# Kernel tuning notes

Hardware: AMD Instinct MI355X
Metric: run time of the kernel (lower is better)

Reference implementation:

```python
import jax, jax.numpy as jnp
import numpy as np

B, D, K = 16384, 4096, 14
EPS = 1e-12  # torch F.normalize eps


def _normalize(x):
    n = jnp.sqrt(jnp.sum(x * x, axis=-1, keepdims=True))
    return x / jnp.maximum(n, EPS)


def setup_inputs() -> dict:
    key = jax.random.key(0)
    ks = jax.random.split(key, 9)
    image_feat = jax.random.normal(ks[0], (B, D), dtype=jnp.float32)
    text_feat = jax.random.normal(ks[1], (B, D), dtype=jnp.float32)
    disease_labels = jax.random.randint(ks[2], (B, K), 0, 2, dtype=jnp.int32)
    # nn.Linear default init: U(-1/sqrt(D), 1/sqrt(D))
    lim = 1.0 / np.sqrt(D)
    Wv = jax.random.uniform(ks[3], (D, D), jnp.float32, -lim, lim)
    bv = jax.random.uniform(ks[4], (D,), jnp.float32, -lim, lim)
    Wt = jax.random.uniform(ks[5], (D, D), jnp.float32, -lim, lim)
    bt = jax.random.uniform(ks[6], (D,), jnp.float32, -lim, lim)
    prototypes = jax.random.normal(ks[7], (K, D), dtype=jnp.float32) * 0.02
    cooccur = np.eye(K, dtype=np.float32)
    for i, j in [(1, 3), (0, 9), (7, 9)]:
        cooccur[i, j] = 0.7
        cooccur[j, i] = 0.7
    cooccurrence = jnp.asarray(cooccur)
    return {
        "image_feat": image_feat, "text_feat": text_feat,
        "disease_labels": disease_labels,
        "Wv": Wv, "bv": bv, "Wt": Wt, "bt": bt,
        "prototypes": prototypes, "cooccurrence": cooccurrence,
    }


def reference(image_feat, text_feat, disease_labels, Wv, bv, Wt, bt, prototypes, cooccurrence):
    labels_f = disease_labels.astype(jnp.float32)  # [B, K]
    v = _normalize(image_feat @ Wv.T + bv)          # [B, D]
    t = _normalize(text_feat @ Wt.T + bt)           # [B, D]
    p = _normalize(prototypes)                      # [K, D]
    v_sim = v @ p.T                                 # [B, K]
    t_sim = t @ p.T                                 # [B, K]
    # Coalition value is linear in the mask and the sampled coalitions differ
    # only at index i, so every Monte Carlo marginal equals this closed form
    # exactly (randomness cancels in value_with - value_without).
    shapley = 0.5 * (v_sim + t_sim) * labels_f      # [B, K]
    batch_cooccur = (labels_f.T @ labels_f) / labels_f.shape[0]  # [K, K]
    learned = jax.nn.sigmoid(cooccurrence)
    cooccur_loss = jnp.mean((learned - jax.lax.stop_gradient(batch_cooccur)) ** 2)
    return shapley, prototypes, cooccur_loss
```

## Files before the change

kernel.cpp:

```cpp
#include <hip/hip_runtime.h>

typedef __bf16 bf16x8 __attribute__((ext_vector_type(8)));
typedef float f32x4 __attribute__((ext_vector_type(4)));
typedef unsigned short u16;
typedef unsigned int u32;

#define D_DIM 4096
#define B_ROWS 16384
#define K_CLS 14
#define M_TOT 32768

__device__ __forceinline__ u32 f2bf(float f) {
    u32 u = __float_as_uint(f);
    return (u + 0x7FFFu + ((u >> 16) & 1u)) >> 16;
}
__device__ __forceinline__ float bfl(u32 u) { return __uint_as_float(u << 16); }
__device__ __forceinline__ float bfh(u32 u) { return __uint_as_float(u & 0xFFFF0000u); }

typedef __attribute__((address_space(3))) void lds_void;
typedef __attribute__((address_space(1))) void glb_void;

__device__ __forceinline__ void g2lds16(const void* g, void* l) {
    __builtin_amdgcn_global_load_lds(
        reinterpret_cast<glb_void*>(reinterpret_cast<uintptr_t>(g)),
        reinterpret_cast<lds_void*>(reinterpret_cast<uintptr_t>(l)),
        16, 0, 0);
}

__global__ void cast_bf16(const float* __restrict__ src, u16* __restrict__ dst, int n4) {
    int i = blockIdx.x * blockDim.x + threadIdx.x;
    int stride = gridDim.x * blockDim.x;
    for (; i < n4; i += stride) {
        float4 a = ((const float4*)src)[i];
        uint2 o;
        o.x = f2bf(a.x) | (f2bf(a.y) << 16);
        o.y = f2bf(a.z) | (f2bf(a.w) << 16);
        ((uint2*)dst)[i] = o;
    }
}

__global__ void proto_norm(const float* __restrict__ P, u16* __restrict__ pTbf,
                           float* __restrict__ outProto) {
    const int k = blockIdx.x;
    const int tid = threadIdx.x;
    float ss = 0.f;
    for (int d = tid; d < D_DIM; d += 256) {
        float v = P[k * D_DIM + d];
        ss += v * v;
    }
    for (int off = 32; off; off >>= 1) ss += __shfl_down(ss, off);
    __shared__ float red[4];
    if ((tid & 63) == 0) red[tid >> 6] = ss;
    __syncthreads();
    float tot = red[0] + red[1] + red[2] + red[3];
    float inv = 1.0f / fmaxf(sqrtf(tot), 1e-12f);
    for (int d = tid; d < D_DIM; d += 256) {
        float v = P[k * D_DIM + d];
        outProto[k * D_DIM + d] = v;
        pTbf[(size_t)d * 16 + k] = (u16)f2bf(v * inv);
    }
}

__global__ void cooccur_bc(const int* __restrict__ L, float* __restrict__ bc) {
    const int i = blockIdx.x / K_CLS, j = blockIdx.x % K_CLS;
    int s = 0;
    for (int b = threadIdx.x; b < B_ROWS; b += 256)
        s += L[b * K_CLS + i] * L[b * K_CLS + j];
    for (int off = 32; off; off >>= 1) s += __shfl_down(s, off);
    __shared__ int red[4];
    if ((threadIdx.x & 63) == 0) red[threadIdx.x >> 6] = s;
    __syncthreads();
    if (threadIdx.x == 0)
        bc[blockIdx.x] = (float)(red[0] + red[1] + red[2] + red[3]) / (float)B_ROWS;
}

__global__ void cooccur_loss(const float* __restrict__ C, const float* __restrict__ bc,
                             float* __restrict__ out) {
    const int t = threadIdx.x;
    float d2 = 0.f;
    if (t < K_CLS * K_CLS) {
        float s = 1.0f / (1.0f + expf(-C[t]));
        float d = s - bc[t];
        d2 = d * d;
    }
    for (int off = 32; off; off >>= 1) d2 += __shfl_down(d2, off);
    __shared__ float red[4];
    if ((t & 63) == 0) red[t >> 6] = d2;
    __syncthreads();
    if (t == 0) out[0] = (red[0] + red[1] + red[2] + red[3]) / (float)(K_CLS * K_CLS);
}

__global__ __launch_bounds__(256) void gemm_bt(
    const u16* __restrict__ Xbf,
    const u16* __restrict__ Wbf,
    const float* __restrict__ bv, const float* __restrict__ bt,
    u16* __restrict__ Ybf)
{
    __shared__ __align__(16) u16 As[128 * 32];
    __shared__ __align__(16) u16 Bs[128 * 32];

    const int tid = threadIdx.x;
    const int wave = tid >> 6, lane = tid & 63;
    const int bn0 = blockIdx.x * 128;
    const int bm0 = blockIdx.y * 128;
    const int half = (bm0 >= B_ROWS) ? 1 : 0;
    const u16* Wsel = Wbf + (size_t)half * D_DIM * D_DIM;
    const float* bias = half ? bt : bv;

    const int srA = lane >> 2;
    const int sc  = (lane & 3) * 8;
    const int g0 = wave * 2, g1 = wave * 2 + 1;
    const u16* Ag = Xbf + (size_t)bm0 * D_DIM;
    const u16* Bg = Wsel + (size_t)bn0 * D_DIM;
    const u16* ga0 = Ag + (size_t)(g0 * 16 + srA) * D_DIM + sc;
    const u16* ga1 = Ag + (size_t)(g1 * 16 + srA) * D_DIM + sc;
    const u16* gb0 = Bg + (size_t)(g0 * 16 + srA) * D_DIM + sc;
    const u16* gb1 = Bg + (size_t)(g1 * 16 + srA) * D_DIM + sc;
    u16* la0 = &As[g0 * 512]; u16* la1 = &As[g1 * 512];
    u16* lb0 = &Bs[g0 * 512]; u16* lb1 = &Bs[g1 * 512];

    const int waveM = wave >> 1, waveN = wave & 1;
    const int mlane = lane & 15, quad = lane >> 4;
    const u16* Ar = &As[(waveM * 64 + mlane) * 32 + quad * 8];
    const u16* Br = &Bs[(waveN * 64 + mlane) * 32 + quad * 8];

    f32x4 acc[4][4] = {};

    for (int k0 = 0; k0 < D_DIM; k0 += 32) {
        __syncthreads();
        g2lds16(ga0 + k0, la0);
        g2lds16(ga1 + k0, la1);
        g2lds16(gb0 + k0, lb0);
        g2lds16(gb1 + k0, lb1);
        __syncthreads();
        bf16x8 a[4], b[4];
#pragma unroll
        for (int mi = 0; mi < 4; mi++) a[mi] = *(const bf16x8*)(Ar + mi * 16 * 32);
#pragma unroll
        for (int ni = 0; ni < 4; ni++) b[ni] = *(const bf16x8*)(Br + ni * 16 * 32);
#pragma unroll
        for (int mi = 0; mi < 4; mi++)
#pragma unroll
            for (int ni = 0; ni < 4; ni++)
                acc[mi][ni] = __builtin_amdgcn_mfma_f32_16x16x32_bf16(
                    a[mi], b[ni], acc[mi][ni], 0, 0, 0);
    }

#pragma unroll
    for (int ni = 0; ni < 4; ni++) {
        const int col = bn0 + waveN * 64 + ni * 16 + mlane;
        const float bcol = bias[col];
#pragma unroll
        for (int mi = 0; mi < 4; mi++) {
            f32x4 v = acc[mi][ni];
#pragma unroll
            for (int r = 0; r < 4; r++) {
                const int row = bm0 + waveM * 64 + mi * 16 + quad * 4 + r;
                Ybf[(size_t)row * D_DIM + col] = (u16)f2bf(v[r] + bcol);
            }
        }
    }
}

__global__ __launch_bounds__(256) void simproj(
    const u16* __restrict__ Ybf, const u16* __restrict__ pTbf,
    float* __restrict__ sim)
{
    const int tid = threadIdx.x;
    const int wave = tid >> 6, lane = tid & 63;
    const int r0 = blockIdx.x * 16 + wave * 4;
    const u16* Y0 = Ybf + (size_t)r0 * D_DIM;

    float acc[4][15];
#pragma unroll
    for (int r = 0; r < 4; r++)
#pragma unroll
        for (int k = 0; k < 15; k++) acc[r][k] = 0.f;

#pragma unroll 2
    for (int i = 0; i < 64; i++) {
        const int d = lane + i * 64;
        const uint4* pq = (const uint4*)(pTbf + (size_t)d * 16);
        const uint4 q0 = pq[0], q1 = pq[1];
        const float p[14] = { bfl(q0.x), bfh(q0.x), bfl(q0.y), bfh(q0.y),
                              bfl(q0.z), bfh(q0.z), bfl(q0.w), bfh(q0.w),
                              bfl(q1.x), bfh(q1.x), bfl(q1.y), bfh(q1.y),
                              bfl(q1.z), bfh(q1.z) };
#pragma unroll
        for (int r = 0; r < 4; r++) {
            const float yv = bfl((u32)Y0[(size_t)r * D_DIM + d]);
            acc[r][14] += yv * yv;
#pragma unroll
            for (int k = 0; k < 14; k++) acc[r][k] += yv * p[k];
        }
    }
#pragma unroll
    for (int r = 0; r < 4; r++)
#pragma unroll
        for (int k = 0; k < 15; k++) {
            float v = acc[r][k];
            v += __shfl_xor(v, 1);  v += __shfl_xor(v, 2);  v += __shfl_xor(v, 4);
            v += __shfl_xor(v, 8);  v += __shfl_xor(v, 16); v += __shfl_xor(v, 32);
            acc[r][k] = v;
        }
    if (lane == 0) {
#pragma unroll
        for (int r = 0; r < 4; r++) {
            const float inv = 1.0f / fmaxf(sqrtf(acc[r][14]), 1e-12f);
#pragma unroll
            for (int k = 0; k < 14; k++)
                sim[(size_t)(r0 + r) * K_CLS + k] = acc[r][k] * inv;
        }
    }
}

__global__ void finalize(const float* __restrict__ sim, const int* __restrict__ L,
                         float* __restrict__ out) {
    const int t = blockIdx.x * 256 + threadIdx.x;
    if (t >= B_ROWS * K_CLS) return;
    out[t] = 0.5f * (sim[t] + sim[t + B_ROWS * K_CLS]) * (float)L[t];
}

extern "C" void kernel_launch(void* const* d_in, const int* in_sizes, int n_in,
                              void* d_out, int out_size, void* d_ws, size_t ws_size,
                              hipStream_t stream) {
    const float* image  = (const float*)d_in[0];
    const float* text   = (const float*)d_in[1];
    const int*   labels = (const int*)d_in[2];
    const float* Wv     = (const float*)d_in[3];
    const float* bv     = (const float*)d_in[4];
    const float* Wt     = (const float*)d_in[5];
    const float* bt     = (const float*)d_in[6];
    const float* protos = (const float*)d_in[7];
    const float* cooc   = (const float*)d_in[8];
    float* out = (float*)d_out;

    const size_t OFF_X   = 0;
    const size_t OFF_W   = 268435456ull;
    const size_t OFF_Y   = 335544320ull;
    const size_t OFF_PT  = 603979776ull;
    const size_t OFF_SIM = 604110848ull;
    const size_t OFF_BC  = 605945856ull;
    const size_t NEED    = 605946640ull;
    if (ws_size < NEED) return;

    char* ws = (char*)d_ws;
    u16*   Xbf  = (u16*)(ws + OFF_X);
    u16*   Wbf  = (u16*)(ws + OFF_W);
    u16*   Ybf  = (u16*)(ws + OFF_Y);
    u16*   pTbf = (u16*)(ws + OFF_PT);
    float* sim  = (float*)(ws + OFF_SIM);
    float* bc   = (float*)(ws + OFF_BC);

    cast_bf16<<<4096, 256, 0, stream>>>(image, Xbf, (B_ROWS * D_DIM) / 4);
    cast_bf16<<<4096, 256, 0, stream>>>(text, Xbf + (size_t)B_ROWS * D_DIM, (B_ROWS * D_DIM) / 4);
    cast_bf16<<<2048, 256, 0, stream>>>(Wv, Wbf, (D_DIM * D_DIM) / 4);
    cast_bf16<<<2048, 256, 0, stream>>>(Wt, Wbf + (size_t)D_DIM * D_DIM, (D_DIM * D_DIM) / 4);

    proto_norm<<<K_CLS, 256, 0, stream>>>(protos, pTbf, out + B_ROWS * K_CLS);
    cooccur_bc<<<K_CLS * K_CLS, 256, 0, stream>>>(labels, bc);
    cooccur_loss<<<1, 256, 0, stream>>>(cooc, bc, out + B_ROWS * K_CLS + K_CLS * D_DIM);

    gemm_bt<<<dim3(D_DIM / 128, M_TOT / 128), 256, 0, stream>>>(Xbf, Wbf, bv, bt, Ybf);

    simproj<<<M_TOT / 16, 256, 0, stream>>>(Ybf, pTbf, sim);

    finalize<<<(B_ROWS * K_CLS + 255) / 256, 256, 0, stream>>>(sim, labels, out);
}
```

Baseline: 1.968 ms.

## Rewrite bf16 GEMM with 256x256 double-buffered tiles and fuse finalize into simproj

The GEMM moves from 128x128 tiles with BK=32, which synchronised twice per k-step, to 256x256 tiles with BK=64 across 8 waves. It double-buffers LDS with async global-to-LDS loads issued two tiles ahead, XOR-swizzles the LDS layout to avoid bank conflicts, and uses setprio-guarded MFMA phases plus a grid swizzle for L2 locality. The aim is to raise arithmetic intensity and hide memory latency behind MFMA work. The simproj kernel now processes image and text rows together and writes the final labelled output directly, which removes the separate finalize kernel and the sim buffer. The larger tile uses 128KB of LDS and more registers, which may limit occupancy.

```diff
diff --git a/kernel.cpp b/kernel.cpp
--- a/kernel.cpp
+++ b/kernel.cpp
@@ -90,86 +90,161 @@
     if (t == 0) out[0] = (red[0] + red[1] + red[2] + red[3]) / (float)(K_CLS * K_CLS);
 }
 
-__global__ __launch_bounds__(256) void gemm_bt(
+#define BK 64
+#define NKT (D_DIM / BK)
+#define TILE_E (256 * 64)
+
+#define STAGE(ABUF, BBUF, k0) do {                                             \
+    _Pragma("unroll")                                                          \
+    for (int i_ = 0; i_ < 4; i_++)                                             \
+        g2lds16(Apan + gOff[i_] + (k0), (ABUF) + lOff[i_]);                    \
+    _Pragma("unroll")                                                          \
+    for (int i_ = 0; i_ < 4; i_++)                                             \
+        g2lds16(Bpan + gOff[i_] + (k0), (BBUF) + lOff[i_]);                    \
+} while (0)
+
+#define LOAD_B(BBUF) do {                                                      \
+    _Pragma("unroll")                                                          \
+    for (int ni_ = 0; ni_ < 4; ni_++) {                                        \
+        bfr[ni_][0] = *(const bf16x8*)((BBUF) + bBase + ni_ * 16 * BK + so0);  \
+        bfr[ni_][1] = *(const bf16x8*)((BBUF) + bBase + ni_ * 16 * BK + so1);  \
+    }                                                                          \
+} while (0)
+
+#define LOAD_A(ABUF, q) do {                                                   \
+    _Pragma("unroll")                                                          \
+    for (int s_ = 0; s_ < 2; s_++) {                                           \
+        afr[s_][0] = *(const bf16x8*)((ABUF) + aBase + ((q) * 32 + s_ * 16) * BK + so0); \
+        afr[s_][1] = *(const bf16x8*)((ABUF) + aBase + ((q) * 32 + s_ * 16) * BK + so1); \
+    }                                                                          \
+} while (0)
+
+#define MFMA_PHASE(q) do {                                                     \
+    __builtin_amdgcn_s_setprio(1);                                             \
+    _Pragma("unroll")                                                          \
+    for (int s_ = 0; s_ < 2; s_++)                                             \
+    _Pragma("unroll")                                                          \
+    for (int ni_ = 0; ni_ < 4; ni_++) {                                        \
+        acc[(q) * 2 + s_][ni_] = __builtin_amdgcn_mfma_f32_16x16x32_bf16(      \
+            afr[s_][0], bfr[ni_][0], acc[(q) * 2 + s_][ni_], 0, 0, 0);         \
+        acc[(q) * 2 + s_][ni_] = __builtin_amdgcn_mfma_f32_16x16x32_bf16(      \
+            afr[s_][1], bfr[ni_][1], acc[(q) * 2 + s_][ni_], 0, 0, 0);         \
+    }                                                                          \
+    __builtin_amdgcn_s_setprio(0);                                             \
+} while (0)
+
+#define PHASE0(ABUF, BBUF) do { LOAD_B(BBUF); LOAD_A(ABUF, 0);                 \
+    __builtin_amdgcn_s_barrier();                                              \
+    asm volatile("s_waitcnt lgkmcnt(0)" ::: "memory");                         \
+    __builtin_amdgcn_sched_barrier(0);                                         \
+    MFMA_PHASE(0);                                                             \
+    __builtin_amdgcn_s_barrier(); } while (0)
+
+#define PHASEQ(ABUF, q) do { LOAD_A(ABUF, q);                                  \
+    __builtin_amdgcn_s_barrier();                                              \
+    asm volatile("s_waitcnt lgkmcnt(0)" ::: "memory");                         \
+    __builtin_amdgcn_sched_barrier(0);                                         \
+    MFMA_PHASE(q);                                                             \
+    __builtin_amdgcn_s_barrier(); } while (0)
+
+#define TILE_BODY(ABUF, BBUF, t) do {                                          \
+    bf16x8 bfr[4][2], afr[2][2];                                               \
+    PHASE0(ABUF, BBUF);                                                        \
+    PHASEQ(ABUF, 1);                                                           \
+    PHASEQ(ABUF, 2);                                                           \
+    PHASEQ(ABUF, 3);                                                           \
+    __builtin_amdgcn_sched_barrier(0);                                         \
+    if ((t) + 2 < NKT) {                                                       \
+        STAGE(ABUF, BBUF, ((t) + 2) * BK);                                     \
+        asm volatile("s_waitcnt vmcnt(8)" ::: "memory");                       \
+    } else if ((t) + 1 < NKT) {                                                \
+        asm volatile("s_waitcnt vmcnt(0)" ::: "memory");                       \
+    }                                                                          \
+    __builtin_amdgcn_sched_barrier(0);                                         \
+    __builtin_amdgcn_s_barrier();                                              \
+} while (0)
+
+__global__ __launch_bounds__(512, 2) void gemm_bt(
     const u16* __restrict__ Xbf,
     const u16* __restrict__ Wbf,
     const float* __restrict__ bv, const float* __restrict__ bt,
     u16* __restrict__ Ybf)
 {
-    __shared__ __align__(16) u16 As[128 * 32];
-    __shared__ __align__(16) u16 Bs[128 * 32];
+    __shared__ __align__(16) u16 lds[4 * TILE_E];
+    u16* const As0 = lds;
+    u16* const As1 = lds + TILE_E;
+    u16* const Bs0 = lds + 2 * TILE_E;
+    u16* const Bs1 = lds + 3 * TILE_E;
 
     const int tid = threadIdx.x;
     const int wave = tid >> 6, lane = tid & 63;
-    const int bn0 = blockIdx.x * 128;
-    const int bm0 = blockIdx.y * 128;
+
+    const int bid = blockIdx.x;
+    const int swzb = (bid & 7) * 256 + (bid >> 3);
+    const int bn0 = (swzb & 15) * 256;
+    const int bm0 = (swzb >> 4) * 256;
     const int half = (bm0 >= B_ROWS) ? 1 : 0;
-    const u16* Wsel = Wbf + (size_t)half * D_DIM * D_DIM;
+    const u16* __restrict__ Apan = Xbf + (size_t)bm0 * D_DIM;
+    const u16* __restrict__ Bpan = Wbf + (size_t)half * D_DIM * D_DIM
+                                       + (size_t)bn0 * D_DIM;
     const float* bias = half ? bt : bv;
 
-    const int srA = lane >> 2;
-    const int sc  = (lane & 3) * 8;
-    const int g0 = wave * 2, g1 = wave * 2 + 1;
-    const u16* Ag = Xbf + (size_t)bm0 * D_DIM;
-    const u16* Bg = Wsel + (size_t)bn0 * D_DIM;
-    const u16* ga0 = Ag + (size_t)(g0 * 16 + srA) * D_DIM + sc;
-    const u16* ga1 = Ag + (size_t)(g1 * 16 + srA) * D_DIM + sc;
-    const u16* gb0 = Bg + (size_t)(g0 * 16 + srA) * D_DIM + sc;
-    const u16* gb1 = Bg + (size_t)(g1 * 16 + srA) * D_DIM + sc;
-    u16* la0 = &As[g0 * 512]; u16* la1 = &As[g1 * 512];
-    u16* lb0 = &Bs[g0 * 512]; u16* lb1 = &Bs[g1 * 512];
-
-    const int waveM = wave >> 1, waveN = wave & 1;
+    const int lrow = lane >> 3;
+    const int lslot = ((lane & 7) ^ lrow) * 8;
+    size_t gOff[4];
+    int lOff[4];
+#pragma unroll
+    for (int i = 0; i < 4; i++) {
+        const int c = wave * 4 + i;
+        gOff[i] = (size_t)(c * 8 + lrow) * D_DIM + lslot;
+        lOff[i] = c * 512;
+    }
+
+    const int wm = wave >> 2, wn = wave & 3;
     const int mlane = lane & 15, quad = lane >> 4;
-    const u16* Ar = &As[(waveM * 64 + mlane) * 32 + quad * 8];
-    const u16* Br = &Bs[(waveN * 64 + mlane) * 32 + quad * 8];
-
-    f32x4 acc[4][4] = {};
-
-    for (int k0 = 0; k0 < D_DIM; k0 += 32) {
-        __syncthreads();
-        g2lds16(ga0 + k0, la0);
-        g2lds16(ga1 + k0, la1);
-        g2lds16(gb0 + k0, lb0);
-        g2lds16(gb1 + k0, lb1);
-        __syncthreads();
-        bf16x8 a[4], b[4];
-#pragma unroll
-        for (int mi = 0; mi < 4; mi++) a[mi] = *(const bf16x8*)(Ar + mi * 16 * 32);
-#pragma unroll
-        for (int ni = 0; ni < 4; ni++) b[ni] = *(const bf16x8*)(Br + ni * 16 * 32);
-#pragma unroll
-        for (int mi = 0; mi < 4; mi++)
-#pragma unroll
-            for (int ni = 0; ni < 4; ni++)
-                acc[mi][ni] = __builtin_amdgcn_mfma_f32_16x16x32_bf16(
-                    a[mi], b[ni], acc[mi][ni], 0, 0, 0);
+    const int lswz = lane & 7;
+    const int so0 = (quad ^ lswz) * 8;
+    const int so1 = ((4 + quad) ^ lswz) * 8;
+    const int aBase = (wm * 128 + mlane) * BK;
+    const int bBase = (wn * 64 + mlane) * BK;
+
+    f32x4 acc[8][4] = {};
+
+    STAGE(As0, Bs0, 0);
+    STAGE(As1, Bs1, BK);
+    asm volatile("s_waitcnt vmcnt(8)" ::: "memory");
+    __builtin_amdgcn_sched_barrier(0);
+    __builtin_amdgcn_s_barrier();
+
+    for (int tt = 0; tt < NKT; tt += 2) {
+        TILE_BODY(As0, Bs0, tt);
+        TILE_BODY(As1, Bs1, tt + 1);
     }
 
 #pragma unroll
     for (int ni = 0; ni < 4; ni++) {
-        const int col = bn0 + waveN * 64 + ni * 16 + mlane;
+        const int col = bn0 + wn * 64 + ni * 16 + mlane;
         const float bcol = bias[col];
 #pragma unroll
-        for (int mi = 0; mi < 4; mi++) {
+        for (int mi = 0; mi < 8; mi++) {
             f32x4 v = acc[mi][ni];
-#pragma unroll
-            for (int r = 0; r < 4; r++) {
-                const int row = bm0 + waveM * 64 + mi * 16 + quad * 4 + r;
-                Ybf[(size_t)row * D_DIM + col] = (u16)f2bf(v[r] + bcol);
-            }
+            const size_t rb = (size_t)(bm0 + wm * 128 + mi * 16 + quad * 4) * D_DIM + col;
+#pragma unroll
+            for (int r = 0; r < 4; r++)
+                Ybf[rb + (size_t)r * D_DIM] = (u16)f2bf(v[r] + bcol);
         }
     }
 }
 
 __global__ __launch_bounds__(256) void simproj(
     const u16* __restrict__ Ybf, const u16* __restrict__ pTbf,
-    float* __restrict__ sim)
+    const int* __restrict__ L, float* __restrict__ out)
 {
     const int tid = threadIdx.x;
     const int wave = tid >> 6, lane = tid & 63;
-    const int r0 = blockIdx.x * 16 + wave * 4;
-    const u16* Y0 = Ybf + (size_t)r0 * D_DIM;
+    const int r0 = blockIdx.x * 8 + wave * 2;
+    const u16* Yi = Ybf + (size_t)r0 * D_DIM;
+    const u16* Yt = Yi + (size_t)B_ROWS * D_DIM;
 
     float acc[4][15];
 #pragma unroll
@@ -186,12 +261,16 @@
                               bfl(q0.z), bfh(q0.z), bfl(q0.w), bfh(q0.w),
                               bfl(q1.x), bfh(q1.x), bfl(q1.y), bfh(q1.y),
                               bfl(q1.z), bfh(q1.z) };
+        float yv[4];
+        yv[0] = bfl((u32)Yi[d]);
+        yv[1] = bfl((u32)Yi[D_DIM + d]);
+        yv[2] = bfl((u32)Yt[d]);
+        yv[3] = bfl((u32)Yt[D_DIM + d]);
 #pragma unroll
         for (int r = 0; r < 4; r++) {
-            const float yv = bfl((u32)Y0[(size_t)r * D_DIM + d]);
-            acc[r][14] += yv * yv;
-#pragma unroll
-            for (int k = 0; k < 14; k++) acc[r][k] += yv * p[k];
+            acc[r][14] += yv[r] * yv[r];
+#pragma unroll
+            for (int k = 0; k < 14; k++) acc[r][k] += yv[r] * p[k];
         }
     }
 #pragma unroll
@@ -205,20 +284,17 @@
         }
     if (lane == 0) {
 #pragma unroll
-        for (int r = 0; r < 4; r++) {
-            const float inv = 1.0f / fmaxf(sqrtf(acc[r][14]), 1e-12f);
-#pragma unroll
-            for (int k = 0; k < 14; k++)
-                sim[(size_t)(r0 + r) * K_CLS + k] = acc[r][k] * inv;
+        for (int rr = 0; rr < 2; rr++) {
+            const float iv = 1.0f / fmaxf(sqrtf(acc[rr][14]), 1e-12f);
+            const float it = 1.0f / fmaxf(sqrtf(acc[2 + rr][14]), 1e-12f);
+#pragma unroll
+            for (int k = 0; k < 14; k++) {
+                const int idx = (r0 + rr) * K_CLS + k;
+                out[idx] = 0.5f * (acc[rr][k] * iv + acc[2 + rr][k] * it)
+                           * (float)L[idx];
+            }
         }
     }
-}
-
-__global__ void finalize(const float* __restrict__ sim, const int* __restrict__ L,
-                         float* __restrict__ out) {
-    const int t = blockIdx.x * 256 + threadIdx.x;
-    if (t >= B_ROWS * K_CLS) return;
-    out[t] = 0.5f * (sim[t] + sim[t + B_ROWS * K_CLS]) * (float)L[t];
 }
 
 extern "C" void kernel_launch(void* const* d_in, const int* in_sizes, int n_in,
@@ -243,13 +319,13 @@
     const size_t OFF_BC  = 605945856ull;
     const size_t NEED    = 605946640ull;
     if (ws_size < NEED) return;
+    (void)OFF_SIM;
 
     char* ws = (char*)d_ws;
     u16*   Xbf  = (u16*)(ws + OFF_X);
     u16*   Wbf  = (u16*)(ws + OFF_W);
     u16*   Ybf  = (u16*)(ws + OFF_Y);
     u16*   pTbf = (u16*)(ws + OFF_PT);
-    float* sim  = (float*)(ws + OFF_SIM);
     float* bc   = (float*)(ws + OFF_BC);
 
     cast_bf16<<<4096, 256, 0, stream>>>(image, Xbf, (B_ROWS * D_DIM) / 4);
@@ -261,9 +337,7 @@
     cooccur_bc<<<K_CLS * K_CLS, 256, 0, stream>>>(labels, bc);
     cooccur_loss<<<1, 256, 0, stream>>>(cooc, bc, out + B_ROWS * K_CLS + K_CLS * D_DIM);
 
-    gemm_bt<<<dim3(D_DIM / 128, M_TOT / 128), 256, 0, stream>>>(Xbf, Wbf, bv, bt, Ybf);
-
-    simproj<<<M_TOT / 16, 256, 0, stream>>>(Ybf, pTbf, sim);
-
-    finalize<<<(B_ROWS * K_CLS + 255) / 256, 256, 0, stream>>>(sim, labels, out);
-}
+    gemm_bt<<<(M_TOT / 256) * (D_DIM / 256), 512, 0, stream>>>(Xbf, Wbf, bv, bt, Ybf);
+
+    simproj<<<B_ROWS / 8, 256, 0, stream>>>(Ybf, pTbf, labels, out);
+}
```

New measurement: 1.888 ms. 1.04x faster.
